# Kernel optimization log

Hardware: AMD Instinct MI355X
Metric: run time of the kernel (lower is better)

The kernel has to match this reference:

```python
import jax, jax.numpy as jnp
import numpy as np

EMBED_DIM = 2048
N_HEADS = 16
N_KV_HEADS = 4
HEAD_DIM = EMBED_DIM // N_HEADS  # 128
NUM_REP = N_HEADS // N_KV_HEADS  # 4
BATCH = 4
SEQLEN = 2048


def setup_inputs() -> dict:
    key = jax.random.key(0)
    kx, kq, kk, kv, ko = jax.random.split(key, 5)
    x = jax.random.normal(kx, (BATCH, SEQLEN, EMBED_DIM), dtype=jnp.float32)
    # Real RoPE table (theta=10000), shape (seqlen, head_dim//2)
    inv_freq = 1.0 / (10000.0 ** (jnp.arange(0, HEAD_DIM, 2, dtype=jnp.float32) / HEAD_DIM))
    t = jnp.arange(SEQLEN, dtype=jnp.float32)
    ang = jnp.outer(t, inv_freq)  # (S, hd/2)
    freqs_cos = jnp.cos(ang)
    freqs_sin = jnp.sin(ang)
    std = 0.02
    wq = jax.random.normal(kq, (EMBED_DIM, N_HEADS * HEAD_DIM), dtype=jnp.float32) * std
    wk = jax.random.normal(kk, (EMBED_DIM, N_KV_HEADS * HEAD_DIM), dtype=jnp.float32) * std
    wv = jax.random.normal(kv, (EMBED_DIM, N_KV_HEADS * HEAD_DIM), dtype=jnp.float32) * std
    wo = jax.random.normal(ko, (N_HEADS * HEAD_DIM, EMBED_DIM), dtype=jnp.float32) * std
    return {"x": x, "freqs_cos": freqs_cos, "freqs_sin": freqs_sin,
            "wq": wq, "wk": wk, "wv": wv, "wo": wo}


def _apply_rope(xh, cos, sin):
    # xh: (b, s, h, hd); cos/sin: (s, hd/2) -> broadcast (1, s, 1, hd/2)
    b, s, h, hd = xh.shape
    xr = xh.reshape(b, s, h, hd // 2, 2)
    x0, x1 = xr[..., 0], xr[..., 1]  # real/imag of complex pairs
    c = cos[None, :, None, :]
    sn = sin[None, :, None, :]
    o0 = x0 * c - x1 * sn
    o1 = x0 * sn + x1 * c
    return jnp.stack([o0, o1], axis=-1).reshape(b, s, h, hd)


def reference(x, freqs_cos, freqs_sin, wq, wk, wv, wo):
    bs, s, _ = x.shape
    xq = (x @ wq).reshape(bs, s, N_HEADS, HEAD_DIM)
    xk = (x @ wk).reshape(bs, s, N_KV_HEADS, HEAD_DIM)
    xv = (x @ wv).reshape(bs, s, N_KV_HEADS, HEAD_DIM)
    xq = _apply_rope(xq, freqs_cos, freqs_sin)
    xk = _apply_rope(xk, freqs_cos, freqs_sin)
    # repeat_kv (GQA): interleave-repeat kv heads to match query heads
    keys = jnp.repeat(xk, NUM_REP, axis=2)    # (b, s, H, hd)
    values = jnp.repeat(xv, NUM_REP, axis=2)
    scale = 1.0 / jnp.sqrt(jnp.float32(HEAD_DIM))
    # SDPA, non-causal
    scores = jnp.einsum('bqhd,bkhd->bhqk', xq, keys) * scale
    probs = jax.nn.softmax(scores, axis=-1)
    out = jnp.einsum('bhqk,bkhd->bqhd', probs, values)
    out = out.reshape(bs, s, N_HEADS * HEAD_DIM)
    return out @ wo
```

## Files before the change

kernel.cpp:

```cpp
#include <hip/hip_runtime.h>
#include <stdint.h>


typedef unsigned short u16;
typedef __bf16 bf16x8 __attribute__((ext_vector_type(8)));
typedef float  f32x4  __attribute__((ext_vector_type(4)));

#define GLOAD16(gp, lp)                                                        \
  __builtin_amdgcn_global_load_lds(                                            \
      (const __attribute__((address_space(1))) void*)(gp),                     \
      (__attribute__((address_space(3))) void*)(lp), 16, 0, 0)

__device__ __forceinline__ u16 f2b(float f) {
  union { float f; uint32_t u; } v; v.f = f;
  uint32_t r = v.u + 0x7FFFu + ((v.u >> 16) & 1u);
  return (u16)(r >> 16);
}
__device__ __forceinline__ float b2f(u16 h) {
  union { uint32_t u; float f; } v; v.u = ((uint32_t)h) << 16;
  return v.f;
}
__device__ __forceinline__ uint2 pack4(float a, float b, float c, float d) {
  uint2 r;
  asm("v_cvt_pk_bf16_f32 %0, %1, %2" : "=v"(r.x) : "v"(a), "v"(b));
  asm("v_cvt_pk_bf16_f32 %0, %1, %2" : "=v"(r.y) : "v"(c), "v"(d));
  return r;
}

__device__ __forceinline__ void bar_sync() {
  asm volatile("s_waitcnt lgkmcnt(0)" ::: "memory");
  __builtin_amdgcn_s_barrier();
  asm volatile("" ::: "memory");
}

__global__ __launch_bounds__(256) void cast_x_kernel(const float4* __restrict__ in,
                                                     ushort4* __restrict__ out) {
  int i = blockIdx.x * 256 + threadIdx.x;
  float4 v = in[i];
  ushort4 o;
  o.x = f2b(v.x); o.y = f2b(v.y); o.z = f2b(v.z); o.w = f2b(v.w);
  out[i] = o;
}

__global__ __launch_bounds__(256) void wtrans_kernel(const float* __restrict__ W,
                                                     u16* __restrict__ WT,
                                                     int K, int N, float scale) {
  __shared__ float t[32][33];
  int n0 = blockIdx.x * 32, k0 = blockIdx.y * 32;
  int tx = threadIdx.x, ty = threadIdx.y;
  for (int r = 0; r < 4; r++)
    t[ty + r * 8][tx] = W[(size_t)(k0 + ty + r * 8) * N + n0 + tx];
  __syncthreads();
  for (int r = 0; r < 4; r++)
    WT[(size_t)(n0 + ty + r * 8) * K + k0 + tx] = f2b(t[tx][ty + r * 8] * scale);
}

template <bool BF16OUT>
__global__ __launch_bounds__(256) void gemm_bt_kernel(const u16* __restrict__ A,
                                                      const u16* __restrict__ BT,
                                                      void* __restrict__ Cv,
                                                      int K, int N) {
  __shared__ u16 As[128 * 32];
  __shared__ u16 Bs[128 * 32];
  const int tid = threadIdx.x;
  const int wave = tid >> 6, lane = tid & 63;
  const int quad = lane >> 4, l16 = lane & 15;
  const int wm = (wave >> 1) * 64, wn = (wave & 1) * 64;
  const size_t m0 = (size_t)blockIdx.y * 128, n0 = (size_t)blockIdx.x * 128;

  f32x4 acc[4][4] = {};
  const int srow = lane >> 2;
  const int scol = (lane & 3) * 8;
  const u16* Ag = A + (m0 + wave * 16 + srow) * (size_t)K + scol;
  const u16* Bg = BT + (n0 + wave * 16 + srow) * (size_t)K + scol;

  for (int k0 = 0; k0 < K; k0 += 32) {
    for (int rd = 0; rd < 2; rd++) {
      GLOAD16(Ag + (size_t)rd * 64 * K + k0, &As[(rd * 64 + wave * 16) * 32]);
      GLOAD16(Bg + (size_t)rd * 64 * K + k0, &Bs[(rd * 64 + wave * 16) * 32]);
    }
    __syncthreads();
    bf16x8 af[4], bf[4];
    for (int i = 0; i < 4; i++)
      af[i] = *(const bf16x8*)&As[(wm + i * 16 + l16) * 32 + quad * 8];
    for (int i = 0; i < 4; i++)
      bf[i] = *(const bf16x8*)&Bs[(wn + i * 16 + l16) * 32 + quad * 8];
    for (int mi = 0; mi < 4; mi++)
      for (int ni = 0; ni < 4; ni++)
        acc[mi][ni] = __builtin_amdgcn_mfma_f32_16x16x32_bf16(af[mi], bf[ni], acc[mi][ni], 0, 0, 0);
    __syncthreads();
  }
  for (int mi = 0; mi < 4; mi++)
    for (int ni = 0; ni < 4; ni++)
      for (int r = 0; r < 4; r++) {
        size_t row = m0 + wm + mi * 16 + quad * 4 + r;
        size_t col = n0 + wn + ni * 16 + l16;
        if (BF16OUT) ((u16*)Cv)[row * N + col] = f2b(acc[mi][ni][r]);
        else         ((float*)Cv)[row * N + col] = acc[mi][ni][r];
      }
}

__global__ __launch_bounds__(256) void rope_kernel(u16* __restrict__ QKV,
                                                   const float* __restrict__ cs,
                                                   const float* __restrict__ sn) {
  int tid = blockIdx.x * 256 + threadIdx.x;
  int row = tid / 1280;
  int p = tid - row * 1280;
  int s = row & 2047;
  int head = p >> 6, i = p & 63;
  u16* ptr = QKV + (size_t)row * 3072 + head * 128 + i * 2;
  unsigned int v = *(unsigned int*)ptr;
  float x0 = b2f((u16)(v & 0xffff)), x1 = b2f((u16)(v >> 16));
  float c = cs[s * 64 + i], ss = sn[s * 64 + i];
  u16 o0 = f2b(x0 * c - x1 * ss);
  u16 o1 = f2b(x0 * ss + x1 * c);
  *(unsigned int*)ptr = (unsigned int)o0 | ((unsigned int)o1 << 16);
}

__global__ __launch_bounds__(256) void vtrans_kernel(const u16* __restrict__ QKV,
                                                     u16* __restrict__ Vt) {
  __shared__ u16 t[32][33];
  int b = blockIdx.z >> 2, hk = blockIdx.z & 3;
  int s0 = blockIdx.x * 32, d0 = blockIdx.y * 32;
  int tx = threadIdx.x, ty = threadIdx.y;
  const u16* src = QKV + (size_t)(b * 2048 + s0) * 3072 + 2560 + hk * 128 + d0;
  for (int r = 0; r < 4; r++)
    t[ty + r * 8][tx] = src[(size_t)(ty + r * 8) * 3072 + tx];
  __syncthreads();
  u16* dst = Vt + ((size_t)((b * 4 + hk) * 128 + d0)) * 2048 + s0;
  for (int r = 0; r < 4; r++)
    dst[(size_t)(ty + r * 8) * 2048 + tx] = t[tx][ty + r * 8];
}

__global__ __launch_bounds__(256, 2) void attn_kernel(const u16* __restrict__ QKV,
                                                      const u16* __restrict__ Vt,
                                                      u16* __restrict__ AO) {
  __shared__ u16 KP[128 * 128];
  __shared__ u16 Vls[128 * 128];
  const int tid = threadIdx.x;
  const int wave = tid >> 6, lane = tid & 63;
  const int quad = lane >> 4, l16 = lane & 15;
  const int qt = blockIdx.x, h = blockIdx.y, b = blockIdx.z;
  const int hk = h >> 2;
  const int sw = l16 & 7;

  bf16x8 qf[2][4];
  {
    const u16* Qb = QKV + (size_t)(b * 2048 + qt * 128 + wave * 32) * 3072 + h * 128;
    for (int qb = 0; qb < 2; qb++)
      for (int ki = 0; ki < 4; ki++)
        qf[qb][ki] = *(const bf16x8*)(Qb + (size_t)(qb * 16 + l16) * 3072 + ki * 32 + quad * 8);
  }
  f32x4 o[8][2] = {};
  float m_[2] = {-1e30f, -1e30f}, l_[2] = {0.f, 0.f};

  const u16* Kg0 = QKV + 2048 + hk * 128;
  const u16* Vg0 = Vt + (size_t)((b * 4 + hk) * 128) * 2048;
  const int r4 = lane >> 4, c16 = lane & 15;

  {
    const u16* Kg = Kg0 + (size_t)(b * 2048) * 3072;
    const u16* Vg = Vg0;
    for (int i = 0; i < 8; i++) {
      int grp = i * 4 + wave;
      int row = grp * 4 + r4;
      int ch = c16 ^ (row & 7);
      GLOAD16(Kg + (size_t)row * 3072 + ch * 8, &KP[grp * 512]);
    }
    for (int i = 0; i < 8; i++) {
      int grp = i * 4 + wave;
      int row = grp * 4 + r4;
      int ch = c16 ^ (row & 7);
      GLOAD16(Vg + (size_t)row * 2048 + ch * 8, &Vls[grp * 512]);
    }
  }
  __syncthreads();

  const int prow = wave * 4 + r4;
  const int pch = c16 ^ (prow & 7);
  const u16* Kpf = Kg0 + ((size_t)(b * 2048 + 128) + prow) * 3072 + pch * 8;
  const int ldsoff = wave * 512 + lane * 8;

  for (int kt = 0; kt < 16; kt++) {
    f32x4 s[8][2];
    for (int kb = 0; kb < 8; kb++) {
      bf16x8 kf[4];
      int a0 = (kb * 16 + l16) * 128 + ((quad ^ sw) << 3);
      for (int ki = 0; ki < 4; ki++)
        kf[ki] = *(const bf16x8*)&KP[a0 ^ (ki * 32)];
      __builtin_amdgcn_s_setprio(1);
      for (int qb = 0; qb < 2; qb++) {
        f32x4 a = {0.f, 0.f, 0.f, 0.f};
        for (int ki = 0; ki < 4; ki++)
          a = __builtin_amdgcn_mfma_f32_16x16x32_bf16(kf[ki], qf[qb][ki], a, 0, 0, 0);
        s[kb][qb] = a;
      }
      __builtin_amdgcn_s_setprio(0);
    }

    uint2 pk[2][8];
    float alch[2];
    for (int qb = 0; qb < 2; qb++) {
      float mk[8];
#pragma unroll
      for (int kb = 0; kb < 8; kb++)
        mk[kb] = fmaxf(fmaxf(s[kb][qb][0], s[kb][qb][1]),
                       fmaxf(s[kb][qb][2], s[kb][qb][3]));
      float mx = fmaxf(fmaxf(fmaxf(mk[0], mk[1]), fmaxf(mk[2], mk[3])),
                       fmaxf(fmaxf(mk[4], mk[5]), fmaxf(mk[6], mk[7])));
      mx = fmaxf(mx, __shfl_xor(mx, 16, 64));
      mx = fmaxf(mx, __shfl_xor(mx, 32, 64));
      float mn = m_[qb], al = 1.0f;
      if (!__all(mx <= m_[qb] + 8.0f)) {
        mn = fmaxf(m_[qb], mx);
        al = exp2f(m_[qb] - mn);
        m_[qb] = mn;
      }
      alch[qb] = al;
      float rs = 0.f;
#pragma unroll
      for (int kb = 0; kb < 8; kb++) {
        float p0 = exp2f(s[kb][qb][0] - mn), p1 = exp2f(s[kb][qb][1] - mn);
        float p2 = exp2f(s[kb][qb][2] - mn), p3 = exp2f(s[kb][qb][3] - mn);
        pk[qb][kb] = pack4(p0, p1, p2, p3);
        rs += (p0 + p1) + (p2 + p3);
      }
      rs += __shfl_xor(rs, 16, 64);
      rs += __shfl_xor(rs, 32, 64);
      l_[qb] = l_[qb] * al + rs;
    }
    if (alch[0] != 1.0f || alch[1] != 1.0f) {
#pragma unroll
      for (int db = 0; db < 8; db++) {
        o[db][0] *= alch[0];
        o[db][1] *= alch[1];
      }
    }

    asm volatile("s_waitcnt vmcnt(0)" ::: "memory");
    asm volatile("s_waitcnt lgkmcnt(0)" ::: "memory");
    __builtin_amdgcn_s_barrier();
    asm volatile("" ::: "memory");

    uint4 kreg[8];
    if (kt < 15) {
#pragma unroll
      for (int i = 0; i < 8; i++)
        kreg[i] = *(const uint4*)(Kpf + (size_t)i * 49152);
    }

    for (int qb = 0; qb < 2; qb++) {
      int rq = wave * 32 + qb * 16 + l16;
      for (int kb = 0; kb < 8; kb++) {
        int ch = (kb * 2 + (quad >> 1)) ^ sw;
        *(uint2*)&KP[rq * 128 + (ch << 3) + (quad & 1) * 4] = pk[qb][kb];
      }
    }
    bf16x8 pf[2][4];
    for (int qb = 0; qb < 2; qb++) {
      int a0 = (wave * 32 + qb * 16 + l16) * 128 + ((quad ^ sw) << 3);
      for (int ki = 0; ki < 4; ki++)
        pf[qb][ki] = *(const bf16x8*)&KP[a0 ^ (ki * 32)];
    }
    for (int db = 0; db < 8; db++) {
      bf16x8 vf[4];
      int a0 = (db * 16 + l16) * 128 + ((quad ^ sw) << 3);
      for (int ki = 0; ki < 4; ki++)
        vf[ki] = *(const bf16x8*)&Vls[a0 ^ (ki * 32)];
      __builtin_amdgcn_s_setprio(1);
      for (int qb = 0; qb < 2; qb++)
        for (int ki = 0; ki < 4; ki++)
          o[db][qb] = __builtin_amdgcn_mfma_f32_16x16x32_bf16(vf[ki], pf[qb][ki], o[db][qb], 0, 0, 0);
      __builtin_amdgcn_s_setprio(0);
    }

    bar_sync();

    if (kt < 15) {
#pragma unroll
      for (int i = 0; i < 8; i++) *(uint4*)&KP[ldsoff + i * 2048] = kreg[i];
      Kpf += 393216;
      __builtin_amdgcn_sched_barrier(0);
      {
        const u16* Vg = Vg0 + (kt + 1) * 128;
        for (int i = 0; i < 8; i++) {
          int grp = i * 4 + wave;
          int row = grp * 4 + r4;
          int ch = c16 ^ (row & 7);
          GLOAD16(Vg + (size_t)row * 2048 + ch * 8, &Vls[grp * 512]);
        }
      }
      bar_sync();
    }
  }

  float inv[2] = {1.0f / l_[0], 1.0f / l_[1]};
  for (int qb = 0; qb < 2; qb++) {
    int rq = wave * 32 + qb * 16 + l16;
    for (int db = 0; db < 8; db++) {
      int ch = (db * 2 + (quad >> 1)) ^ sw;
      uint2 pv = pack4(o[db][qb][0] * inv[qb], o[db][qb][1] * inv[qb],
                       o[db][qb][2] * inv[qb], o[db][qb][3] * inv[qb]);
      *(uint2*)&KP[rq * 128 + (ch << 3) + (quad & 1) * 4] = pv;
    }
  }
  __syncthreads();
  u16* Ab = AO + (size_t)(b * 2048 + qt * 128) * 2048 + h * 128;
  for (int i = 0; i < 8; i++) {
    int row = i * 16 + (tid >> 4);
    int seg = tid & 15;
    int pc = seg ^ (row & 7);
    *(uint4*)(Ab + (size_t)row * 2048 + seg * 8) = *(const uint4*)&KP[row * 128 + pc * 8];
  }
}

extern "C" void kernel_launch(void* const* d_in, const int* in_sizes, int n_in,
                              void* d_out, int out_size, void* d_ws, size_t ws_size,
                              hipStream_t stream) {
  (void)in_sizes; (void)n_in; (void)out_size; (void)ws_size;
  const float* x    = (const float*)d_in[0];
  const float* fcos = (const float*)d_in[1];
  const float* fsin = (const float*)d_in[2];
  const float* wq   = (const float*)d_in[3];
  const float* wk   = (const float*)d_in[4];
  const float* wv   = (const float*)d_in[5];
  const float* wo   = (const float*)d_in[6];

  char* w = (char*)d_ws;
  u16* xb  = (u16*)w;
  u16* wT  = (u16*)(w + 33554432);
  u16* woT = (u16*)(w + 33554432 + 12582912);
  u16* QKV = (u16*)(w + 33554432 + 12582912 + 8388608);
  u16* Vt  = (u16*)(w + 33554432 + 12582912 + 8388608 + 50331648);
  u16* AO  = xb;

  const float C = 0.08838834764831845f * 1.44269504088896340f;

  cast_x_kernel<<<16384, 256, 0, stream>>>((const float4*)x, (ushort4*)xb);
  wtrans_kernel<<<dim3(64, 64), dim3(32, 8), 0, stream>>>(wq, wT, 2048, 2048, C);
  wtrans_kernel<<<dim3(16, 64), dim3(32, 8), 0, stream>>>(wk, wT + (size_t)2048 * 2048, 2048, 512, 1.0f);
  wtrans_kernel<<<dim3(16, 64), dim3(32, 8), 0, stream>>>(wv, wT + (size_t)2560 * 2048, 2048, 512, 1.0f);
  wtrans_kernel<<<dim3(64, 64), dim3(32, 8), 0, stream>>>(wo, woT, 2048, 2048, 1.0f);

  gemm_bt_kernel<true><<<dim3(24, 64), 256, 0, stream>>>(xb, wT, QKV, 2048, 3072);
  rope_kernel<<<40960, 256, 0, stream>>>(QKV, fcos, fsin);
  vtrans_kernel<<<dim3(64, 4, 16), dim3(32, 8), 0, stream>>>(QKV, Vt);
  attn_kernel<<<dim3(16, 16, 4), 256, 0, stream>>>(QKV, Vt, AO);
  gemm_bt_kernel<false><<<dim3(16, 64), 256, 0, stream>>>(AO, woT, (float*)d_out, 2048, 2048);
}
```

Before: 667.7 us.

## Build P fragments via ds_bpermute and stream next K tile during softmax

Replaces the LDS round-trip used to transpose the softmax probabilities into MFMA B-operand layout with in-register cross-lane ds_bpermute shuffles. This frees the K buffer right after QK^T, so the next K tile is issued with direct global-to-LDS loads during softmax instead of being staged through registers. V loads are moved to the start of each iteration and the waits are narrowed with partial vmcnt counts. The bpermute traffic and the new barrier placement add their own latency, and the partial vmcnt(8) wait depends on the exact ordering of outstanding loads.

```diff
diff --git a/kernel.cpp b/kernel.cpp
--- a/kernel.cpp
+++ b/kernel.cpp
@@ -158,30 +158,36 @@
   const u16* Vg0 = Vt + (size_t)((b * 4 + hk) * 128) * 2048;
   const int r4 = lane >> 4, c16 = lane & 15;
 
-  {
-    const u16* Kg = Kg0 + (size_t)(b * 2048) * 3072;
-    const u16* Vg = Vg0;
+  auto stageK = [&](int t) {
+    const u16* Kg = Kg0 + (size_t)(b * 2048 + t * 128) * 3072;
     for (int i = 0; i < 8; i++) {
       int grp = i * 4 + wave;
       int row = grp * 4 + r4;
       int ch = c16 ^ (row & 7);
       GLOAD16(Kg + (size_t)row * 3072 + ch * 8, &KP[grp * 512]);
     }
+  };
+  auto stageV = [&](int t) {
+    const u16* Vg = Vg0 + t * 128;
     for (int i = 0; i < 8; i++) {
       int grp = i * 4 + wave;
       int row = grp * 4 + r4;
       int ch = c16 ^ (row & 7);
       GLOAD16(Vg + (size_t)row * 2048 + ch * 8, &Vls[grp * 512]);
     }
-  }
+  };
+
+  stageK(0);
+  stageV(0);
   __syncthreads();
 
-  const int prow = wave * 4 + r4;
-  const int pch = c16 ^ (prow & 7);
-  const u16* Kpf = Kg0 + ((size_t)(b * 2048 + 128) + prow) * 3072 + pch * 8;
-  const int ldsoff = wave * 512 + lane * 8;
+  const int bpA = (((quad & 1) << 5) + l16) << 2;
+  const int bpB = bpA + 64;
+  const bool hi = quad >= 2;
 
   for (int kt = 0; kt < 16; kt++) {
+    if (kt > 0) stageV(kt);
+
     f32x4 s[8][2];
     for (int kb = 0; kb < 8; kb++) {
       bf16x8 kf[4];
@@ -198,7 +204,10 @@
       __builtin_amdgcn_s_setprio(0);
     }
 
-    uint2 pk[2][8];
+    bar_sync();
+    if (kt < 15) stageK(kt + 1);
+
+    bf16x8 pf[2][4];
     float alch[2];
     for (int qb = 0; qb < 2; qb++) {
       float mk[8];
@@ -217,17 +226,37 @@
         m_[qb] = mn;
       }
       alch[qb] = al;
+      uint2 u[8];
       float rs = 0.f;
 #pragma unroll
       for (int kb = 0; kb < 8; kb++) {
         float p0 = exp2f(s[kb][qb][0] - mn), p1 = exp2f(s[kb][qb][1] - mn);
         float p2 = exp2f(s[kb][qb][2] - mn), p3 = exp2f(s[kb][qb][3] - mn);
-        pk[qb][kb] = pack4(p0, p1, p2, p3);
+        u[kb] = pack4(p0, p1, p2, p3);
         rs += (p0 + p1) + (p2 + p3);
       }
       rs += __shfl_xor(rs, 16, 64);
       rs += __shfl_xor(rs, 32, 64);
       l_[qb] = l_[qb] * al + rs;
+#pragma unroll
+      for (int ki = 0; ki < 4; ki++) {
+        int Ax = (int)u[2 * ki].x, Ay = (int)u[2 * ki].y;
+        int Bx = (int)u[2 * ki + 1].x, By = (int)u[2 * ki + 1].y;
+        int pAx = __builtin_amdgcn_ds_bpermute(bpA, Ax);
+        int pBx = __builtin_amdgcn_ds_bpermute(bpA, Bx);
+        int pAy = __builtin_amdgcn_ds_bpermute(bpA, Ay);
+        int pBy = __builtin_amdgcn_ds_bpermute(bpA, By);
+        int qAx = __builtin_amdgcn_ds_bpermute(bpB, Ax);
+        int qBx = __builtin_amdgcn_ds_bpermute(bpB, Bx);
+        int qAy = __builtin_amdgcn_ds_bpermute(bpB, Ay);
+        int qBy = __builtin_amdgcn_ds_bpermute(bpB, By);
+        uint4 d;
+        d.x = hi ? (uint32_t)pBx : (uint32_t)pAx;
+        d.y = hi ? (uint32_t)pBy : (uint32_t)pAy;
+        d.z = hi ? (uint32_t)qBx : (uint32_t)qAx;
+        d.w = hi ? (uint32_t)qBy : (uint32_t)qAy;
+        pf[qb][ki] = *(bf16x8*)&d;
+      }
     }
     if (alch[0] != 1.0f || alch[1] != 1.0f) {
 #pragma unroll
@@ -237,31 +266,10 @@
       }
     }
 
-    asm volatile("s_waitcnt vmcnt(0)" ::: "memory");
-    asm volatile("s_waitcnt lgkmcnt(0)" ::: "memory");
-    __builtin_amdgcn_s_barrier();
-    asm volatile("" ::: "memory");
-
-    uint4 kreg[8];
-    if (kt < 15) {
-#pragma unroll
-      for (int i = 0; i < 8; i++)
-        kreg[i] = *(const uint4*)(Kpf + (size_t)i * 49152);
-    }
-
-    for (int qb = 0; qb < 2; qb++) {
-      int rq = wave * 32 + qb * 16 + l16;
-      for (int kb = 0; kb < 8; kb++) {
-        int ch = (kb * 2 + (quad >> 1)) ^ sw;
-        *(uint2*)&KP[rq * 128 + (ch << 3) + (quad & 1) * 4] = pk[qb][kb];
-      }
-    }
-    bf16x8 pf[2][4];
-    for (int qb = 0; qb < 2; qb++) {
-      int a0 = (wave * 32 + qb * 16 + l16) * 128 + ((quad ^ sw) << 3);
-      for (int ki = 0; ki < 4; ki++)
-        pf[qb][ki] = *(const bf16x8*)&KP[a0 ^ (ki * 32)];
-    }
+    if (kt == 15) asm volatile("s_waitcnt vmcnt(0)" ::: "memory");
+    else          asm volatile("s_waitcnt vmcnt(8)" ::: "memory");
+    bar_sync();
+
     for (int db = 0; db < 8; db++) {
       bf16x8 vf[4];
       int a0 = (db * 16 + l16) * 128 + ((quad ^ sw) << 3);
@@ -274,24 +282,8 @@
       __builtin_amdgcn_s_setprio(0);
     }
 
+    asm volatile("s_waitcnt vmcnt(0)" ::: "memory");
     bar_sync();
-
-    if (kt < 15) {
-#pragma unroll
-      for (int i = 0; i < 8; i++) *(uint4*)&KP[ldsoff + i * 2048] = kreg[i];
-      Kpf += 393216;
-      __builtin_amdgcn_sched_barrier(0);
-      {
-        const u16* Vg = Vg0 + (kt + 1) * 128;
-        for (int i = 0; i < 8; i++) {
-          int grp = i * 4 + wave;
-          int row = grp * 4 + r4;
-          int ch = c16 ^ (row & 7);
-          GLOAD16(Vg + (size_t)row * 2048 + ch * 8, &Vls[grp * 512]);
-        }
-      }
-      bar_sync();
-    }
   }
 
   float inv[2] = {1.0f / l_[0], 1.0f / l_[1]};
```

After: 618.1 us. -7.4%, faster.
